# Kernel tuning notes

Measured on AMD Instinct MI355X. Metric: run time of the kernel, lower is better.

The kernel has to match this reference:

```python
import jax, jax.numpy as jnp
import numpy as np

EPS = 1e-6
NUM_HEADS = 12


def ln_cf(x, w, b):
    # channels_first LayerNorm over channel dim (ConvNeXt style)
    u = jnp.mean(x, axis=1, keepdims=True)
    s = jnp.mean((x - u) ** 2, axis=1, keepdims=True)
    xn = (x - u) / jnp.sqrt(s + EPS)
    shp = (1, -1) + (1,) * (x.ndim - 2)
    return xn * w.reshape(shp) + b.reshape(shp)


def conv2s2(x, w):
    # Conv3d kernel=2 stride=2 (no bias): exact non-overlapping patch contraction
    b, c, H, W, D = x.shape
    xp = x.reshape(b, c, H // 2, 2, W // 2, 2, D // 2, 2)
    return jnp.einsum('bchkwpdq,ockpq->bohwd', xp, w)


def convt2s2(x, w):
    # ConvTranspose3d kernel=2 stride=2 (torch weight layout [in, out, 2,2,2])
    b, i, H, W, D = x.shape
    o = w.shape[1]
    y = jnp.einsum('bihwd,iokpq->bohkwpdq', x, w)
    return y.reshape(b, o, 2 * H, 2 * W, 2 * D)


def stem(x, w1, g1, b1, w2, g2, b2):
    h = conv2s2(x, w1)
    h = jax.nn.gelu(ln_cf(h, g1, b1), approximate=False)
    h = conv2s2(h, w2)
    return ln_cf(h, g2, b2)


def debed(x, tw1, g, b, tw2, tb2):
    h = convt2s2(x, tw1)
    h = jax.nn.gelu(ln_cf(h, g, b), approximate=False)
    return convt2s2(h, tw2) + tb2.reshape(1, -1, 1, 1, 1)


def rope(x):
    # rotary embedding over full token dim c (pairs (i, i+c/2)), positions 0..L-1
    b, l, c = x.shape
    inv = 1.0 / (10000.0 ** (jnp.arange(0, c, 2, dtype=jnp.float32) / c))
    t = jnp.arange(l, dtype=jnp.float32)
    f = jnp.outer(t, inv)                      # [l, c/2]
    emb = jnp.concatenate([f, f], axis=-1)     # [l, c]
    cos, sin = jnp.cos(emb)[None], jnp.sin(emb)[None]
    rot = jnp.concatenate([-x[..., c // 2:], x[..., :c // 2]], axis=-1)
    return x * cos + rot * sin


def _forward(x, skip, q_w1, q_g1, q_b1, q_w2, q_g2, q_b2,
             k_w1, k_g1, k_b1, k_w2, k_g2, k_b2,
             v_w1, v_g1, v_b1, v_w2, v_g2, v_b2,
             o_tw1, o_g, o_b, o_tw2, o_tb2,
             ns_w, ns_b, nx_w, nx_b, no_w, no_b):
    res = skip
    skip = ln_cf(skip, ns_w, ns_b)
    x = ln_cf(x, nx_w, nx_b)
    q = stem(skip, q_w1, q_g1, q_b1, q_w2, q_g2, q_b2)
    k = stem(x, k_w1, k_g1, k_b1, k_w2, k_g2, k_b2)
    v = stem(x, v_w1, v_g1, v_b1, v_w2, v_g2, v_b2)
    b, c, Hq, Wq, Dq = q.shape
    _, _, Hk, Wk, Dk = k.shape
    q = q.reshape(b, c, -1).transpose(0, 2, 1)   # [b, Lq, c]
    k = k.reshape(b, c, -1).transpose(0, 2, 1)   # [b, Lk, c]
    v = v.reshape(b, c, -1).transpose(0, 2, 1)
    q = rope(q)
    k = rope(k)
    hd = c // NUM_HEADS
    qh = q.reshape(b, -1, NUM_HEADS, hd).transpose(0, 2, 1, 3)  # [b, nh, Lq, hd]
    kh = k.reshape(b, -1, NUM_HEADS, hd).transpose(0, 2, 1, 3)
    vh = v.reshape(b, -1, NUM_HEADS, hd).transpose(0, 2, 1, 3)
    scale = 1.0 / jnp.sqrt(jnp.float32(hd))
    attn = jax.nn.softmax(jnp.einsum('bhqc,bhkc->bhqk', qh, kh) * scale, axis=-1)
    proj = jnp.einsum('bhqk,bhkc->bhqc', attn, vh)              # [b, nh, Lq, hd]
    # rearrange 'b nh l c -> b (c nh) h w d'
    proj = proj.transpose(0, 3, 1, 2).reshape(b, c, Hq, Wq, Dq)
    proj = ln_cf(proj, no_w, no_b)
    out = debed(proj, o_tw1, o_g, o_b, o_tw2, o_tb2)
    return out + res


def setup_inputs() -> dict:
    key = jax.random.key(0)
    ks = iter(jax.random.split(key, 40))
    def nrm(shape, scale):
        return jax.random.normal(next(ks), shape, jnp.float32) * scale
    E, E4, XF, SF = 768, 192, 6, 6
    inp = {
        'x': nrm((2, XF, 48, 48, 48), 1.0),
        'skip': nrm((2, SF, 48, 48, 48), 1.0),
    }
    for p, ic in [('q', SF), ('k', XF), ('v', XF)]:
        inp[p + '_w1'] = nrm((E4, ic, 2, 2, 2), (ic * 8) ** -0.5)
        inp[p + '_g1'] = jnp.ones(E4, jnp.float32)
        inp[p + '_b1'] = jnp.zeros(E4, jnp.float32)
        inp[p + '_w2'] = nrm((E, E4, 2, 2, 2), (E4 * 8) ** -0.5)
        inp[p + '_g2'] = jnp.ones(E, jnp.float32)
        inp[p + '_b2'] = jnp.zeros(E, jnp.float32)
    inp['o_tw1'] = nrm((E, E4, 2, 2, 2), E ** -0.5)
    inp['o_g'] = jnp.ones(E4, jnp.float32)
    inp['o_b'] = jnp.zeros(E4, jnp.float32)
    inp['o_tw2'] = nrm((E4, SF, 2, 2, 2), E4 ** -0.5)
    inp['o_tb2'] = jnp.zeros(SF, jnp.float32)
    inp['ns_w'] = jnp.ones(SF, jnp.float32)
    inp['ns_b'] = jnp.zeros(SF, jnp.float32)
    inp['nx_w'] = jnp.ones(XF, jnp.float32)
    inp['nx_b'] = jnp.zeros(XF, jnp.float32)
    inp['no_w'] = jnp.ones(E, jnp.float32)
    inp['no_b'] = jnp.zeros(E, jnp.float32)
    return inp


def reference(x, skip, q_w1, q_g1, q_b1, q_w2, q_g2, q_b2,
              k_w1, k_g1, k_b1, k_w2, k_g2, k_b2,
              v_w1, v_g1, v_b1, v_w2, v_g2, v_b2,
              o_tw1, o_g, o_b, o_tw2, o_tb2,
              ns_w, ns_b, nx_w, nx_b, no_w, no_b):
    return _forward(x, skip, q_w1, q_g1, q_b1, q_w2, q_g2, q_b2,
                    k_w1, k_g1, k_b1, k_w2, k_g2, k_b2,
                    v_w1, v_g1, v_b1, v_w2, v_g2, v_b2,
                    o_tw1, o_g, o_b, o_tw2, o_tb2,
                    ns_w, ns_b, nx_w, nx_b, no_w, no_b)
```

## Files before the change

### kernel.cpp

```cpp
#include <hip/hip_runtime.h>
#include <math.h>

#define BB_ 2
#define C0 6
#define S0 48
#define V0 (S0*S0*S0)
#define C1 192
#define S1 24
#define V1 (S1*S1*S1)
#define C2 768
#define S2 12
#define LL (S2*S2*S2)
#define NH 12
#define HD 64
#define KDIM (C1*8)
#define MDIM (BB_*LL)

typedef __attribute__((ext_vector_type(8))) short short8;
typedef __attribute__((ext_vector_type(4))) short short4v;
typedef __attribute__((ext_vector_type(4))) float float4v;

static __device__ __forceinline__ float gelu_exact(float x){
  return 0.5f*x*(1.0f+erff(x*0.70710678118654752440f));
}
static __device__ __forceinline__ unsigned short f2bf(float f){
  unsigned int u = __float_as_uint(f);
  unsigned int r = (u + 0x7fffu + ((u>>16)&1u)) >> 16;
  return (unsigned short)r;
}
static __device__ __forceinline__ unsigned int pk_bf16(float a, float b){
#if __has_builtin(__builtin_amdgcn_cvt_pk_bf16_f32)
  typedef __attribute__((ext_vector_type(2))) __bf16 bf2;
  bf2 r = __builtin_amdgcn_cvt_pk_bf16_f32(a,b);
  union { bf2 v; unsigned int u; } cv; cv.v = r;
  return cv.u;
#else
  return (unsigned int)f2bf(a) | ((unsigned int)f2bf(b)<<16);
#endif
}
static __device__ __forceinline__ float bf2f(unsigned short u){
  return __uint_as_float(((unsigned int)u)<<16);
}
static __device__ __forceinline__ float exp2v(float x){
#if __has_builtin(__builtin_amdgcn_exp2f)
  return __builtin_amdgcn_exp2f(x);
#else
  return exp2f(x);
#endif
}
static __device__ __forceinline__ void load_lds16(const void* g, void* l){
  __builtin_amdgcn_global_load_lds((const __attribute__((address_space(1))) unsigned int*)g,
      (__attribute__((address_space(3))) unsigned int*)l, 16, 0, 0);
}
static __device__ __forceinline__ float4v mfma32(short8 a, short8 b, float4v c){
  return __builtin_amdgcn_mfma_f32_16x16x32_bf16(a,b,c,0,0,0);
}
static __device__ __forceinline__ float4v mfma16(short4v a, short4v b, float4v c){
#if __has_builtin(__builtin_amdgcn_mfma_f32_16x16x16bf16_1k)
  return __builtin_amdgcn_mfma_f32_16x16x16bf16_1k(a,b,c,0,0,0);
#else
  asm volatile("v_mfma_f32_16x16x16_bf16 %0, %1, %2, %0" : "+v"(c) : "v"(a), "v"(b));
  return c;
#endif
}

__global__ __launch_bounds__(256) void prep_kernel(
    const float* __restrict__ skin, const float* __restrict__ xin,
    const float* __restrict__ nsw, const float* __restrict__ nsb,
    const float* __restrict__ nxw, const float* __restrict__ nxb,
    unsigned short* __restrict__ outS, unsigned short* __restrict__ outX,
    const float* __restrict__ qw2, const float* __restrict__ kw2, const float* __restrict__ vw2,
    const float* __restrict__ tw1, const float* __restrict__ tw2,
    const float* __restrict__ qw1, const float* __restrict__ kw1, const float* __restrict__ vw1,
    unsigned short* __restrict__ w2tq, unsigned short* __restrict__ w2tk,
    unsigned short* __restrict__ w2tv, unsigned short* __restrict__ Btd,
    unsigned short* __restrict__ Bt48,
    unsigned short* __restrict__ w1q, unsigned short* __restrict__ w1k,
    unsigned short* __restrict__ w1v){
  int bx = blockIdx.x;
  if (bx < 1728){
    int z = bx >= 864;
    const float* in = z ? xin : skin;
    const float* w  = z ? nxw : nsw;
    const float* bi = z ? nxb : nsb;
    unsigned short* out = z ? outX : outS;
    int idx = (bx - z*864)*256 + threadIdx.x;
    int b = idx / V0, vox = idx - b*V0;
    const float* p = in + (size_t)b*(C0*V0) + vox;
    float v[C0]; float s=0.f;
#pragma unroll
    for (int c=0;c<C0;c++){ v[c]=p[(size_t)c*V0]; s+=v[c]; }
    float u = s*(1.f/C0);
    float ss=0.f;
#pragma unroll
    for (int c=0;c<C0;c++){ float d=v[c]-u; ss+=d*d; }
    float inv = rsqrtf(ss*(1.f/C0)+1e-6f);
    unsigned short* o = out + (size_t)b*(C0*V0) + vox;
#pragma unroll
    for (int c=0;c<C0;c++) o[(size_t)c*V0] = f2bf((v[c]-u)*inv*w[c]+bi[c]);
    return;
  }
  bx -= 1728;
  if (bx < 13824){
    int z = bx/4608;
    int idx = (bx - z*4608)*256 + threadIdx.x;
    const float* w2 = (z==0)?qw2:((z==1)?kw2:vw2);
    unsigned short* o = (z==0)?w2tq:((z==1)?w2tk:w2tv);
    int oc = idx/KDIM; int r = idx-oc*KDIM; int p = r/C1; int ic = r-p*C1;
    o[idx] = f2bf(w2[(size_t)oc*KDIM + ic*8 + p]);
  } else if (bx < 18432){
    int idx = (bx-13824)*256 + threadIdx.x;
    int n = idx/C2; int p = idx-n*C2;
    int i = ((p&63)*NH) + (p>>6);
    int kpq = n/C1, o2 = n-kpq*C1;
    Btd[idx] = f2bf(tw1[(size_t)i*KDIM + o2*8 + kpq]);
  } else if (bx < 18480){
    int idx = (bx-18432)*256 + threadIdx.x;
    int n = idx/C1; int i = idx-n*C1;
    Bt48[idx] = (n<48) ? f2bf(tw2[(size_t)i*48 + n]) : (unsigned short)0;
  } else {
    int idx = (bx-18480)*256 + threadIdx.x;
    int z = idx / 9216; int r = idx - z*9216;
    const float* w1 = (z==0)?qw1:((z==1)?kw1:vw1);
    unsigned short* o = (z==0)?w1q:((z==1)?w1k:w1v);
    o[r] = f2bf(w1[r]);
  }
}

__global__ __launch_bounds__(256) void conv1_kernel(
    const unsigned short* __restrict__ lnSb, const unsigned short* __restrict__ lnXb,
    const unsigned short* __restrict__ w1bq, const unsigned short* __restrict__ w1bk,
    const unsigned short* __restrict__ w1bv,
    const float* __restrict__ qg1, const float* __restrict__ qb1,
    const float* __restrict__ kg1, const float* __restrict__ kb1,
    const float* __restrict__ vg1, const float* __restrict__ vb1,
    unsigned short* __restrict__ h1q, unsigned short* __restrict__ h1k,
    unsigned short* __restrict__ h1v){
  int z = blockIdx.z;
  const unsigned short* in = (z==0)? lnSb : lnXb;
  const unsigned short* Wb = (z==0)?w1bq:((z==1)?w1bk:w1bv);
  const float* g1 = (z==0)?qg1:((z==1)?kg1:vg1);
  const float* b1 = (z==0)?qb1:((z==1)?kb1:vb1);
  unsigned short* h1p = (z==0)?h1q:((z==1)?h1k:h1v);
  int t = threadIdx.x, w = t>>6, lane = t&63;
  int g = lane>>4, l16 = lane&15;
  int j = blockIdx.x*4 + w;
  int bxh = j/18, mt = j - bxh*18;
  int b = bxh/48; int rem = bxh - b*48; int y = rem>>1, xh = rem&1;
  int xo = mt/3, zo = mt - xo*3;
  int xv = xh*12 + xo*2 + (l16>>3);
  int zv = zo*8 + (l16&7);
  int x2 = 2*xv, z2 = 2*zv, y2 = 2*y;
  const unsigned short* base = in + (size_t)b*C0*V0;
  union { short8 v; unsigned int u[4]; } aA;
  {
    size_t rb = (size_t)g*V0;
    aA.u[0] = *(const unsigned int*)&base[rb + (y2+0)*(S0*S0) + (x2+0)*S0 + z2];
    aA.u[1] = *(const unsigned int*)&base[rb + (y2+0)*(S0*S0) + (x2+1)*S0 + z2];
    aA.u[2] = *(const unsigned int*)&base[rb + (y2+1)*(S0*S0) + (x2+0)*S0 + z2];
    aA.u[3] = *(const unsigned int*)&base[rb + (y2+1)*(S0*S0) + (x2+1)*S0 + z2];
  }
  union { short4v v; unsigned int u[2]; } aB;
  {
    size_t rb = (size_t)(4+(g>>1))*V0 + (y2+(g&1))*(S0*S0);
    aB.u[0] = *(const unsigned int*)&base[rb + (x2+0)*S0 + z2];
    aB.u[1] = *(const unsigned int*)&base[rb + (x2+1)*S0 + z2];
  }
  float4v acc[12];
#pragma unroll
  for (int ot=0; ot<12; ot++){
    short8  wA = *(const short8*)&Wb[(ot*16+l16)*48 + g*8];
    short4v wB = *(const short4v*)&Wb[(ot*16+l16)*48 + 32 + g*4];
    float4v a = {};
    a = mfma32(wA, aA.v, a);
    a = mfma16(wB, aB.v, a);
    acc[ot] = a;
  }
  float s1=0.f, s2=0.f;
#pragma unroll
  for (int ot=0;ot<12;ot++)
#pragma unroll
    for (int reg=0;reg<4;reg++){ float v=acc[ot][reg]; s1+=v; s2+=v*v; }
  s1 += __shfl_xor(s1,16); s1 += __shfl_xor(s1,32);
  s2 += __shfl_xor(s2,16); s2 += __shfl_xor(s2,32);
  float u = s1*(1.f/C1);
  float inv = rsqrtf(s2*(1.f/C1)-u*u+1e-6f);
  int tok = (y>>1)*(S2*S2) + (xv>>1)*S2 + (zv>>1);
  int p8 = (y&1)*4 + (xv&1)*2 + (zv&1);
  unsigned short* hb = h1p + (size_t)(b*LL+tok)*KDIM + p8*C1;
#pragma unroll
  for (int ot=0; ot<12; ot++){
    int oc0 = ot*16 + g*4;
    float4 gg = *(const float4*)&g1[oc0];
    float4 bb = *(const float4*)&b1[oc0];
    float x0 = gelu_exact((acc[ot][0]-u)*inv*gg.x+bb.x);
    float x1 = gelu_exact((acc[ot][1]-u)*inv*gg.y+bb.y);
    float x2e= gelu_exact((acc[ot][2]-u)*inv*gg.z+bb.z);
    float x3 = gelu_exact((acc[ot][3]-u)*inv*gg.w+bb.w);
    uint2 pk; pk.x = pk_bf16(x0,x1); pk.y = pk_bf16(x2e,x3);
    *(uint2*)&hb[oc0] = pk;
  }
}

__global__ __launch_bounds__(256) void gemm_stem_kernel(
    const unsigned short* __restrict__ A0, const unsigned short* __restrict__ A1,
    const unsigned short* __restrict__ A2,
    const unsigned short* __restrict__ B0, const unsigned short* __restrict__ B1,
    const unsigned short* __restrict__ B2,
    unsigned short* __restrict__ Cq, unsigned short* __restrict__ Ck,
    unsigned short* __restrict__ Cv){
  int flat = blockIdx.x;
  int xcd = flat & 7, slot = flat >> 3;
  int tile = xcd*122 + slot;
  if (tile >= 972) return;
  int z = tile/324; int rr = tile - z*324;
  int m0 = (rr/12)*128, n0 = (rr - (rr/12)*12)*64;
  const unsigned short* A = (z==0)?A0:((z==1)?A1:A2);
  const unsigned short* Bt = (z==0)?B0:((z==1)?B1:B2);
  unsigned short* Cp = (z==0)?Cq:((z==1)?Ck:Cv);
  __shared__ __align__(16) unsigned short Al[2][128*32];
  __shared__ __align__(16) unsigned short Bl[2][64*32];
  int t=threadIdx.x, w=t>>6, lane=t&63;
  int g=lane>>4, l16=lane&15, r16=lane>>2, c16=lane&3;
  int wm=w>>1, wn=w&1;
  int csrc = (c16 ^ ((r16>>1)&3))*8;
  int crd  = (g   ^ ((l16>>1)&3))*8;
  float4v acc[4][2] = {};
#pragma unroll
  for (int cc=0;cc<3;cc++){
    int ch = w*3+cc;
    if (ch<8) load_lds16(A + (size_t)(m0+ch*16+r16)*KDIM + csrc, &Al[0][ch*512]);
    else      load_lds16(Bt + (size_t)(n0+(ch-8)*16+r16)*KDIM + csrc, &Bl[0][(ch-8)*512]);
  }
  __syncthreads();
  int cur = 0;
  for (int kb=0;kb<KDIM;kb+=32){
    if (kb+32 < KDIM){
      int nb = cur^1;
#pragma unroll
      for (int cc=0;cc<3;cc++){
        int ch = w*3+cc;
        if (ch<8) load_lds16(A + (size_t)(m0+ch*16+r16)*KDIM + (kb+32) + csrc, &Al[nb][ch*512]);
        else      load_lds16(Bt + (size_t)(n0+(ch-8)*16+r16)*KDIM + (kb+32) + csrc, &Bl[nb][(ch-8)*512]);
      }
    }
    short8 af[4], bf[2];
#pragma unroll
    for (int mt=0;mt<4;mt++) af[mt] = *(const short8*)&Al[cur][(wm*64+mt*16+l16)*32 + crd];
#pragma unroll
    for (int nt=0;nt<2;nt++) bf[nt] = *(const short8*)&Bl[cur][(wn*32+nt*16+l16)*32 + crd];
#pragma unroll
    for (int mt=0;mt<4;mt++)
#pragma unroll
      for (int nt=0;nt<2;nt++)
        acc[mt][nt] = mfma32(af[mt], bf[nt], acc[mt][nt]);
    __syncthreads();
    cur ^= 1;
  }
#pragma unroll
  for (int mt=0;mt<4;mt++){
    int mb = m0 + wm*64 + mt*16 + g*4;
#pragma unroll
    for (int nt=0;nt<2;nt++){
      int col = n0 + wn*32 + nt*16 + l16;
#pragma unroll
      for (int reg=0;reg<4;reg++)
        Cp[(size_t)(mb+reg)*C2 + col] = f2bf(acc[mt][nt][reg]);
    }
  }
}

__global__ __launch_bounds__(256) void gemm_debed_kernel(const unsigned short* __restrict__ A,
    const unsigned short* __restrict__ Bt, unsigned short* __restrict__ C){
  int flat = blockIdx.x;
  int xcd = flat & 7, slot = flat >> 3;
  int tile = xcd*81 + slot;
  int m0 = (tile/24)*128, n0 = (tile - (tile/24)*24)*64;
  __shared__ __align__(16) unsigned short Al[2][128*32];
  __shared__ __align__(16) unsigned short Bl[2][64*32];
  int t=threadIdx.x, w=t>>6, lane=t&63;
  int g=lane>>4, l16=lane&15, r16=lane>>2, c16=lane&3;
  int wm=w>>1, wn=w&1;
  int csrc = (c16 ^ ((r16>>1)&3))*8;
  int crd  = (g   ^ ((l16>>1)&3))*8;
  float4v acc[4][2] = {};
#pragma unroll
  for (int cc=0;cc<3;cc++){
    int ch = w*3+cc;
    if (ch<8) load_lds16(A + (size_t)(m0+ch*16+r16)*C2 + csrc, &Al[0][ch*512]);
    else      load_lds16(Bt + (size_t)(n0+(ch-8)*16+r16)*C2 + csrc, &Bl[0][(ch-8)*512]);
  }
  __syncthreads();
  int cur = 0;
  for (int kb=0;kb<C2;kb+=32){
    if (kb+32 < C2){
      int nb = cur^1;
#pragma unroll
      for (int cc=0;cc<3;cc++){
        int ch = w*3+cc;
        if (ch<8) load_lds16(A + (size_t)(m0+ch*16+r16)*C2 + (kb+32) + csrc, &Al[nb][ch*512]);
        else      load_lds16(Bt + (size_t)(n0+(ch-8)*16+r16)*C2 + (kb+32) + csrc, &Bl[nb][(ch-8)*512]);
      }
    }
    short8 af[4], bf[2];
#pragma unroll
    for (int mt=0;mt<4;mt++) af[mt] = *(const short8*)&Al[cur][(wm*64+mt*16+l16)*32 + crd];
#pragma unroll
    for (int nt=0;nt<2;nt++) bf[nt] = *(const short8*)&Bl[cur][(wn*32+nt*16+l16)*32 + crd];
#pragma unroll
    for (int mt=0;mt<4;mt++)
#pragma unroll
      for (int nt=0;nt<2;nt++)
        acc[mt][nt] = mfma32(af[mt], bf[nt], acc[mt][nt]);
    __syncthreads();
    cur ^= 1;
  }
#pragma unroll
  for (int nt=0;nt<2;nt++){
    int n = n0 + wn*32 + nt*16 + l16;
    int kpq = n / C1;
    int o = n - kpq*C1;
#pragma unroll
    for (int mt=0;mt<4;mt++){
      int mb = m0 + wm*64 + mt*16 + g*4;
#pragma unroll
      for (int reg=0;reg<4;reg++){
        int m = mb + reg;
        int b = m / LL; int tok = m - b*LL;
        int h = tok/(S2*S2), ww=(tok/S2)%S2, d=tok%S2;
        int v24 = (2*h+((kpq>>2)&1))*(S1*S1) + (2*ww+((kpq>>1)&1))*S1 + (2*d+(kpq&1));
        C[(size_t)(b*V1+v24)*C1 + o] = f2bf(acc[mt][nt][reg]);
      }
    }
  }
}

__global__ __launch_bounds__(256) void final_kernel(const unsigned short* __restrict__ dh,
    const unsigned short* __restrict__ Bt48, const float* __restrict__ og,
    const float* __restrict__ ob, const float* __restrict__ tb2s,
    const float* __restrict__ skipp, float* __restrict__ out){
  __shared__ __align__(16) unsigned short As[64*200];
  __shared__ __align__(16) unsigned short Bs[64*200];
  int t=threadIdx.x, w=t>>6, lane=t&63;
  int g=lane>>4, l16=lane&15;
  int m0 = blockIdx.x*64;
  for (int n8 = t; n8 < 1536; n8 += 256){
    int n64 = n8/24, kk = (n8 - n64*24)*8;
    uint4 d4 = *(const uint4*)&Bt48[n64*192 + kk];
    *(uint4*)&Bs[n64*200 + kk] = d4;
  }
  float g0=og[lane], g1v=og[lane+64], g2v=og[lane+128];
  float b0=ob[lane], b1v=ob[lane+64], b2v=ob[lane+128];
  for (int rr=0; rr<16; rr++){
    int rl = w*16 + rr;
    const unsigned short* row = dh + (size_t)(m0+rl)*C1;
    float v0=bf2f(row[lane]), v1=bf2f(row[lane+64]), v2=bf2f(row[lane+128]);
    float s1=v0+v1+v2, s2=v0*v0+v1*v1+v2*v2;
#pragma unroll
    for (int off=32;off>0;off>>=1){ s1+=__shfl_xor(s1,off); s2+=__shfl_xor(s2,off); }
    float u=s1*(1.f/C1), inv=rsqrtf(s2*(1.f/C1)-u*u+1e-6f);
    As[rl*200+lane]     = f2bf(gelu_exact((v0-u)*inv*g0+b0));
    As[rl*200+lane+64]  = f2bf(gelu_exact((v1-u)*inv*g1v+b1v));
    As[rl*200+lane+128] = f2bf(gelu_exact((v2-u)*inv*g2v+b2v));
  }
  __syncthreads();
  int wm=w>>1, wn=w&1;
  float4v acc[2][2] = {};
#pragma unroll
  for (int kb=0;kb<192;kb+=32){
    short8 af[2], bf[2];
#pragma unroll
    for (int mt=0;mt<2;mt++) af[mt] = *(const short8*)&As[(wm*32+mt*16+l16)*200 + kb + g*8];
#pragma unroll
    for (int nt=0;nt<2;nt++) bf[nt] = *(const short8*)&Bs[(wn*32+nt*16+l16)*200 + kb + g*8];
#pragma unroll
    for (int mt=0;mt<2;mt++)
#pragma unroll
      for (int nt=0;nt<2;nt++)
        acc[mt][nt] = mfma32(af[mt], bf[nt], acc[mt][nt]);
  }
#pragma unroll
  for (int nt=0;nt<2;nt++){
    int n = wn*32 + nt*16 + l16;
    if (n < 48){
      int c = n>>3, kpq = n&7;
      float bias = tb2s[c];
#pragma unroll
      for (int mt=0;mt<2;mt++){
        int mb = m0 + wm*32 + mt*16 + g*4;
#pragma unroll
        for (int reg=0;reg<4;reg++){
          int m = mb + reg;
          int b = m / V1; int v24 = m - b*V1;
          int y24 = v24/(S1*S1), x24=(v24/S1)%S1, z24=v24%S1;
          int vox = (2*y24+((kpq>>2)&1))*(S0*S0) + (2*x24+((kpq>>1)&1))*S0 + 2*z24+(kpq&1);
          size_t oi = (size_t)(b*C0+c)*V0 + vox;
          out[oi] = acc[mt][nt][reg] + bias + skipp[oi];
        }
      }
    }
  }
}

__global__ __launch_bounds__(256) void ln768_stem_kernel(
    unsigned short* __restrict__ qb, unsigned short* __restrict__ kb2,
    unsigned short* __restrict__ vb,
    const float* __restrict__ qg, const float* __restrict__ qbi,
    const float* __restrict__ kg, const float* __restrict__ kbi,
    const float* __restrict__ vg, const float* __restrict__ vbi, float qscale){
  int z = blockIdx.y;
  unsigned short* buf = (z==0)?qb:((z==1)?kb2:vb);
  const float* g  = (z==0)?qg:((z==1)?kg:vg);
  const float* bia= (z==0)?qbi:((z==1)?kbi:vbi);
  float scale = (z==0)? qscale : 1.0f;
  int tok = blockIdx.x*4 + (threadIdx.x>>6), lane = threadIdx.x&63;
  unsigned short* row = buf + (size_t)tok*C2;
  float v[12]; float s1=0.f,s2=0.f;
#pragma unroll
  for (int i=0;i<12;i++){ float t=bf2f(row[i*64+lane]); v[i]=t; s1+=t; s2+=t*t; }
#pragma unroll
  for (int off=32;off>0;off>>=1){ s1+=__shfl_xor(s1,off); s2+=__shfl_xor(s2,off); }
  float u=s1*(1.f/C2);
  float inv=rsqrtf(s2*(1.f/C2)-u*u+1e-6f);
  if (z==2){
#pragma unroll
    for (int i=0;i<12;i++){ int j=i*64+lane; row[j]=f2bf((v[i]-u)*inv*g[j]+bia[j]); }
  } else {
    int pos = tok % LL;
#pragma unroll
    for (int i=0;i<6;i++){
      int j=i*64+lane;
      float xn1=(v[i]-u)*inv*g[j]+bia[j];
      float xn2=(v[i+6]-u)*inv*g[j+384]+bia[j+384];
      float fr=(float)pos*__expf(-0.02398526139f*(float)j);
      float cs=cosf(fr), sn=sinf(fr);
      row[j]     = f2bf((xn1*cs - xn2*sn)*scale);
      row[j+384] = f2bf((xn2*cs + xn1*sn)*scale);
    }
  }
}

__global__ __launch_bounds__(256) void vtrans_kernel(const unsigned short* __restrict__ vbf,
    unsigned short* __restrict__ vT){
  __shared__ unsigned short T[64*72];
  int tok0 = blockIdx.x*64;
  int h = blockIdx.y, b = blockIdx.z;
  int t = threadIdx.x;
#pragma unroll
  for (int i=0;i<2;i++){
    int idx = t + i*256;
    int token = idx>>3, dc = idx&7;
    uint4 d4 = *(const uint4*)&vbf[(size_t)(b*LL+tok0+token)*C2 + h*64 + dc*8];
    const unsigned short* s = (const unsigned short*)&d4;
#pragma unroll
    for (int j2=0;j2<8;j2++) T[(dc*8+j2)*72 + token] = s[j2];
  }
  __syncthreads();
  int r = t>>2, seg = t&3;
  unsigned short* dst = vT + (size_t)((b*NH+h)*HD + r)*LL + tok0 + seg*16;
  uint4 o[2];
  unsigned short* os = (unsigned short*)o;
#pragma unroll
  for (int j2=0;j2<16;j2++) os[j2] = T[r*72 + seg*16 + j2];
  *(uint4*)dst = o[0];
  *(uint4*)(dst+8) = o[1];
}

__global__ __launch_bounds__(256) void attn_kernel(const unsigned short* __restrict__ q,
    const unsigned short* __restrict__ k, const unsigned short* __restrict__ vt,
    unsigned short* __restrict__ opart, float* __restrict__ lbuf){
  __shared__ __align__(16) unsigned char smem[32768];
  unsigned short* Ks = (unsigned short*)smem;
  unsigned short* Vs = Ks + 4096;
  int flat = blockIdx.x;
  int xcd = flat & 7, slot = flat >> 3;
  int tile = xcd*108 + slot;
  int h = tile / 72; int rem = tile - h*72;
  int zb = rem / 9, qt = rem - zb*9;
  int b = zb >> 2, split = zb & 3;
  int t=threadIdx.x, w=t>>6, lane=t&63;
  int g=lane>>4, l16=lane&15;
  short8 qA[3], qB[3];
#pragma unroll
  for (int j=0;j<3;j++){
    const unsigned short* qrow = q + (size_t)(b*LL + qt*192 + w*48 + j*16 + l16)*C2 + h*64;
    qA[j] = *(const short8*)(qrow + g*8);
    qB[j] = *(const short8*)(qrow + 32 + g*8);
  }
  const unsigned short* kbase = k + (size_t)(b*LL)*C2 + h*64;
  const unsigned short* vbase = vt + (size_t)((b*NH+h)*HD)*LL;
  int sub = lane>>3;
  int chs = (lane&7) ^ sub;
  int ktb = split*7, kte = (split==3)? 27 : (split*7+7);
  const unsigned short* gptr[4];
  unsigned short* ldst[4];
  int gstep[4];
#pragma unroll
  for (int cc=0;cc<4;cc++){
    int ii = w*4+cc;
    if (ii<8){
      int key = ktb*64 + ii*8 + sub;
      gptr[cc] = kbase + (size_t)key*C2 + chs*8;
      gstep[cc] = 64*C2;
      ldst[cc] = &Ks[ii*512];
    } else {
      int d = (ii-8)*8 + sub;
      gptr[cc] = vbase + (size_t)d*LL + ktb*64 + chs*8;
      gstep[cc] = 64;
      ldst[cc] = &Vs[(ii-8)*512];
    }
  }
  int sw = l16 & 7;
  const unsigned short* ksrow = &Ks[l16*64 + (g^sw)*8];
  int c2d = (((4+g)^sw) - (g^sw))*8;
  const unsigned short* vsrow = &Vs[l16*64 + (g&1)*4];
  int xk[4];
#pragma unroll
  for (int kc=0;kc<4;kc++) xk[kc] = (((kc*2 + (g>>1)) ^ sw))*8;
  short4v vones;
  vones[0]=vones[1]=vones[2]=vones[3]=(short)0x3F80;
  float4v O4[3][4] = {};
  float4v Ol[3] = {};
#pragma unroll
  for (int cc=0;cc<4;cc++){
    load_lds16(gptr[cc], ldst[cc]);
    gptr[cc] += gstep[cc];
  }
  __syncthreads();
  int cur = 0;
  for (int kt=ktb; kt<kte; kt++){
    if (kt+1 < kte){
      int so = (cur^1)*8192;
#pragma unroll
      for (int cc=0;cc<4;cc++){
        load_lds16(gptr[cc], ldst[cc]+so);
        gptr[cc] += gstep[cc];
      }
    }
    int co = cur*8192;
    const unsigned short* kr = ksrow + co;
    const unsigned short* vr = vsrow + co;
    float4v sc[3][4];
#pragma unroll
    for (int nt=0;nt<4;nt++){
      short8 k1 = *(const short8*)(kr + nt*1024);
      short8 k2 = *(const short8*)(kr + nt*1024 + c2d);
#pragma unroll
      for (int j=0;j<3;j++){
        float4v zz = {};
        zz = mfma32(k1, qA[j], zz);
        zz = mfma32(k2, qB[j], zz);
        sc[j][nt] = zz;
      }
    }
#pragma unroll
    for (int j=0;j<3;j++)
#pragma unroll
      for (int nt=0;nt<4;nt++)
#pragma unroll
        for (int reg=0;reg<4;reg++)
          sc[j][nt][reg] = exp2v(sc[j][nt][reg]);
    short4v pbs[3][4];
#pragma unroll
    for (int j=0;j<3;j++)
#pragma unroll
      for (int kc=0;kc<4;kc++){
        union { short4v v; unsigned int u[2]; } pb;
        pb.u[0] = pk_bf16(sc[j][kc][0], sc[j][kc][1]);
        pb.u[1] = pk_bf16(sc[j][kc][2], sc[j][kc][3]);
        pbs[j][kc] = pb.v;
      }
#pragma unroll
    for (int kc=0;kc<4;kc++){
      const unsigned short* vp = vr + xk[kc];
      short4v va[4];
#pragma unroll
      for (int dt=0;dt<4;dt++) va[dt] = *(const short4v*)(vp + dt*1024);
#pragma unroll
      for (int j=0;j<3;j++){
        Ol[j] = mfma16(vones, pbs[j][kc], Ol[j]);
#pragma unroll
        for (int dt=0;dt<4;dt++)
          O4[j][dt] = mfma16(va[dt], pbs[j][kc], O4[j][dt]);
      }
    }
    __syncthreads();
    cur ^= 1;
  }
  float* Ot = (float*)smem;
  float* ot = Ot + w*1216;
  int qq = lane>>2, c4 = lane&3;
#pragma unroll
  for (int j=0;j<3;j++){
#pragma unroll
    for (int dt=0;dt<4;dt++)
      *(float4*)&ot[l16*76 + dt*16 + g*4] =
          make_float4(O4[j][dt][0],O4[j][dt][1],O4[j][dt][2],O4[j][dt][3]);
    if (g==0){
      int qi = qt*192 + w*48 + j*16 + l16;
      lbuf[((size_t)(b*4+split)*NH+h)*LL + qi] = Ol[j][0];
    }
    unsigned short* orow = opart + (size_t)split*MDIM*C2
                + (size_t)(b*LL + qt*192 + w*48 + j*16 + qq)*C2 + h*64;
#pragma unroll
    for (int p=0;p<4;p++){
      float4 vv = *(float4*)&ot[qq*76 + p*16 + c4*4];
      uint2 pk; pk.x = pk_bf16(vv.x,vv.y); pk.y = pk_bf16(vv.z,vv.w);
      *(uint2*)&orow[p*16 + c4*4] = pk;
    }
    __syncthreads();
  }
}

__global__ __launch_bounds__(256) void attn_post_kernel(const unsigned short* __restrict__ opart,
    const float* __restrict__ lbuf,
    const float* __restrict__ g, const float* __restrict__ bia,
    unsigned short* __restrict__ aob){
  int t=threadIdx.x, w=t>>6, lane=t&63;
  int m = blockIdx.x*4 + w;
  int b = m / LL, l = m - b*LL;
  const unsigned short* o0 = opart + (size_t)m*C2;
  unsigned short* orow = aob + (size_t)m*C2;
  float vv[12]; float s1=0.f, s2=0.f;
#pragma unroll
  for (int i=0;i<12;i++){
    float ls = 0.f;
#pragma unroll
    for (int s=0;s<4;s++) ls += lbuf[((size_t)(b*4+s)*NH+i)*LL + l];
    float inv = 1.f/ls;
    int j = i*64+lane;
    float val = 0.f;
#pragma unroll
    for (int s=0;s<4;s++) val += bf2f(o0[(size_t)s*MDIM*C2 + j]);
    val *= inv;
    vv[i]=val; s1+=val; s2+=val*val;
  }
#pragma unroll
  for (int off=32;off>0;off>>=1){ s1+=__shfl_xor(s1,off); s2+=__shfl_xor(s2,off); }
  float u=s1*(1.f/C2);
  float invs=rsqrtf(s2*(1.f/C2)-u*u+1e-6f);
#pragma unroll
  for (int i=0;i<12;i++){
    int cj = lane*NH + i;
    orow[i*64+lane] = f2bf((vv[i]-u)*invs*g[cj]+bia[cj]);
  }
}

extern "C" void kernel_launch(void* const* d_in, const int* in_sizes, int n_in,
                              void* d_out, int out_size, void* d_ws, size_t ws_size,
                              hipStream_t stream){
  (void)in_sizes; (void)n_in; (void)out_size; (void)ws_size;
  const float* x    =(const float*)d_in[0];
  const float* skip =(const float*)d_in[1];
  const float* q_w1 =(const float*)d_in[2];
  const float* q_g1 =(const float*)d_in[3];
  const float* q_b1 =(const float*)d_in[4];
  const float* q_w2 =(const float*)d_in[5];
  const float* q_g2 =(const float*)d_in[6];
  const float* q_b2 =(const float*)d_in[7];
  const float* k_w1 =(const float*)d_in[8];
  const float* k_g1 =(const float*)d_in[9];
  const float* k_b1 =(const float*)d_in[10];
  const float* k_w2 =(const float*)d_in[11];
  const float* k_g2 =(const float*)d_in[12];
  const float* k_b2 =(const float*)d_in[13];
  const float* v_w1 =(const float*)d_in[14];
  const float* v_g1 =(const float*)d_in[15];
  const float* v_b1 =(const float*)d_in[16];
  const float* v_w2 =(const float*)d_in[17];
  const float* v_g2 =(const float*)d_in[18];
  const float* v_b2 =(const float*)d_in[19];
  const float* o_tw1=(const float*)d_in[20];
  const float* o_g  =(const float*)d_in[21];
  const float* o_b  =(const float*)d_in[22];
  const float* o_tw2=(const float*)d_in[23];
  const float* o_tb2=(const float*)d_in[24];
  const float* ns_w =(const float*)d_in[25];
  const float* ns_b =(const float*)d_in[26];
  const float* nx_w =(const float*)d_in[27];
  const float* nx_b =(const float*)d_in[28];
  const float* no_w =(const float*)d_in[29];
  const float* no_b =(const float*)d_in[30];
  float* out=(float*)d_out;

  char* W = (char*)d_ws;
  unsigned short* lnSb = (unsigned short*)(W + 0);
  unsigned short* lnXb = (unsigned short*)(W + 2654208);
  unsigned short* h1q  = (unsigned short*)(W + 5308416);
  unsigned short* h1k  = (unsigned short*)(W + 15925248);
  unsigned short* h1v  = (unsigned short*)(W + 26542080);
  unsigned short* w2tq = (unsigned short*)(W + 37158912);
  unsigned short* w2tk = (unsigned short*)(W + 39518208);
  unsigned short* w2tv = (unsigned short*)(W + 41877504);
  unsigned short* qbf  = (unsigned short*)(W + 44236800);
  unsigned short* kbf  = (unsigned short*)(W + 49545216);
  unsigned short* vbf  = (unsigned short*)(W + 54853632);
  unsigned short* vT   = (unsigned short*)(W + 60162048);
  unsigned short* aob  = (unsigned short*)(W + 65470464);
  unsigned short* Btd  = (unsigned short*)(W + 70778880);
  unsigned short* Bt48 = (unsigned short*)(W + 73138176);
  unsigned short* w1q  = (unsigned short*)(W + 73162752);
  unsigned short* w1k  = (unsigned short*)(W + 73181184);
  unsigned short* w1v  = (unsigned short*)(W + 73199616);
  float* lbuf  = (float*)(W + 0);
  unsigned short* opart = (unsigned short*)(W + 5308416);
  unsigned short* dh   = (unsigned short*)(W + 5308416);

  const float QSCALE = 0.125f*1.44269504089f;

  prep_kernel<<<20316,256,0,stream>>>(skip, x, ns_w, ns_b, nx_w, nx_b, lnSb, lnXb,
      q_w2,k_w2,v_w2,o_tw1,o_tw2, q_w1,k_w1,v_w1,
      w2tq,w2tk,w2tv,Btd,Bt48, w1q,w1k,w1v);
  conv1_kernel<<<dim3(432,1,3),256,0,stream>>>(lnSb,lnXb, w1q,w1k,w1v,
      q_g1,q_b1, k_g1,k_b1, v_g1,v_b1, h1q,h1k,h1v);
  gemm_stem_kernel<<<976,256,0,stream>>>(h1q,h1k,h1v,
      w2tq,w2tk,w2tv, qbf,kbf,vbf);
  ln768_stem_kernel<<<dim3(864,3),256,0,stream>>>(qbf,kbf,vbf,
      q_g2,q_b2, k_g2,k_b2, v_g2,v_b2, QSCALE);
  vtrans_kernel<<<dim3(27,12,2),256,0,stream>>>(vbf, vT);
  attn_kernel<<<864,256,0,stream>>>(qbf, kbf, vT, opart, lbuf);
  attn_post_kernel<<<864,256,0,stream>>>(opart, lbuf, no_w, no_b, aob);
  gemm_debed_kernel<<<648,256,0,stream>>>(aob, Btd, dh);
  final_kernel<<<432,256,0,stream>>>(dh, Bt48, o_g, o_b, o_tb2, skip, out);
}
```

Baseline: 326.3 us.

## Triple-buffer LDS staging in stem and debed GEMMs with vmcnt-based waits

Both the stem and debed bf16 GEMM kernels move from double-buffered to triple-buffered LDS tiles. The global-to-LDS load for a tile two steps ahead is issued before the current tile's MFMAs. Each iteration now waits with s_waitcnt vmcnt(3) plus a raw s_barrier instead of a full __syncthreads that drains all loads. This keeps one tile of loads in flight across the barrier to hide global latency, at the cost of 50% more LDS per block (possibly lowering occupancy) and reliance on exact vmcnt counting.

```diff
diff --git a/kernel.cpp b/kernel.cpp
--- a/kernel.cpp
+++ b/kernel.cpp
@@ -218,45 +218,58 @@
   const unsigned short* A = (z==0)?A0:((z==1)?A1:A2);
   const unsigned short* Bt = (z==0)?B0:((z==1)?B1:B2);
   unsigned short* Cp = (z==0)?Cq:((z==1)?Ck:Cv);
-  __shared__ __align__(16) unsigned short Al[2][128*32];
-  __shared__ __align__(16) unsigned short Bl[2][64*32];
+  __shared__ __align__(16) unsigned short Al[3][128*32];
+  __shared__ __align__(16) unsigned short Bl[3][64*32];
   int t=threadIdx.x, w=t>>6, lane=t&63;
   int g=lane>>4, l16=lane&15, r16=lane>>2, c16=lane&3;
   int wm=w>>1, wn=w&1;
   int csrc = (c16 ^ ((r16>>1)&3))*8;
   int crd  = (g   ^ ((l16>>1)&3))*8;
   float4v acc[4][2] = {};
-#pragma unroll
-  for (int cc=0;cc<3;cc++){
-    int ch = w*3+cc;
-    if (ch<8) load_lds16(A + (size_t)(m0+ch*16+r16)*KDIM + csrc, &Al[0][ch*512]);
-    else      load_lds16(Bt + (size_t)(n0+(ch-8)*16+r16)*KDIM + csrc, &Bl[0][(ch-8)*512]);
-  }
-  __syncthreads();
-  int cur = 0;
-  for (int kb=0;kb<KDIM;kb+=32){
-    if (kb+32 < KDIM){
-      int nb = cur^1;
-#pragma unroll
-      for (int cc=0;cc<3;cc++){
-        int ch = w*3+cc;
-        if (ch<8) load_lds16(A + (size_t)(m0+ch*16+r16)*KDIM + (kb+32) + csrc, &Al[nb][ch*512]);
-        else      load_lds16(Bt + (size_t)(n0+(ch-8)*16+r16)*KDIM + (kb+32) + csrc, &Bl[nb][(ch-8)*512]);
-      }
-    }
+  auto STAGE = [&](int buf, int kcol){
+#pragma unroll
+    for (int cc=0;cc<3;cc++){
+      int ch = w*3+cc;
+      if (ch<8) load_lds16(A + (size_t)(m0+ch*16+r16)*KDIM + kcol + csrc, &Al[buf][ch*512]);
+      else      load_lds16(Bt + (size_t)(n0+(ch-8)*16+r16)*KDIM + kcol + csrc, &Bl[buf][(ch-8)*512]);
+    }
+  };
+  auto COMPUTE = [&](int buf){
     short8 af[4], bf[2];
 #pragma unroll
-    for (int mt=0;mt<4;mt++) af[mt] = *(const short8*)&Al[cur][(wm*64+mt*16+l16)*32 + crd];
-#pragma unroll
-    for (int nt=0;nt<2;nt++) bf[nt] = *(const short8*)&Bl[cur][(wn*32+nt*16+l16)*32 + crd];
+    for (int mt=0;mt<4;mt++) af[mt] = *(const short8*)&Al[buf][(wm*64+mt*16+l16)*32 + crd];
+#pragma unroll
+    for (int nt=0;nt<2;nt++) bf[nt] = *(const short8*)&Bl[buf][(wn*32+nt*16+l16)*32 + crd];
 #pragma unroll
     for (int mt=0;mt<4;mt++)
 #pragma unroll
       for (int nt=0;nt<2;nt++)
         acc[mt][nt] = mfma32(af[mt], bf[nt], acc[mt][nt]);
-    __syncthreads();
-    cur ^= 1;
-  }
+  };
+  const int NT = KDIM/32;
+  STAGE(0, 0);
+  STAGE(1, 32);
+  asm volatile("s_waitcnt vmcnt(3)" ::: "memory");
+  __builtin_amdgcn_s_barrier();
+  __builtin_amdgcn_sched_barrier(0);
+  int cur = 0;
+  for (int tt=0; tt<NT-2; tt++){
+    int nb = cur+2; if (nb>=3) nb-=3;
+    STAGE(nb, tt*32+64);
+    COMPUTE(cur);
+    __builtin_amdgcn_sched_barrier(0);
+    asm volatile("s_waitcnt vmcnt(3)" ::: "memory");
+    __builtin_amdgcn_s_barrier();
+    __builtin_amdgcn_sched_barrier(0);
+    cur++; if (cur>=3) cur-=3;
+  }
+  COMPUTE(cur);
+  __builtin_amdgcn_sched_barrier(0);
+  asm volatile("s_waitcnt vmcnt(0)" ::: "memory");
+  __builtin_amdgcn_s_barrier();
+  __builtin_amdgcn_sched_barrier(0);
+  cur++; if (cur>=3) cur-=3;
+  COMPUTE(cur);
 #pragma unroll
   for (int mt=0;mt<4;mt++){
     int mb = m0 + wm*64 + mt*16 + g*4;
@@ -276,45 +289,58 @@
   int xcd = flat & 7, slot = flat >> 3;
   int tile = xcd*81 + slot;
   int m0 = (tile/24)*128, n0 = (tile - (tile/24)*24)*64;
-  __shared__ __align__(16) unsigned short Al[2][128*32];
-  __shared__ __align__(16) unsigned short Bl[2][64*32];
+  __shared__ __align__(16) unsigned short Al[3][128*32];
+  __shared__ __align__(16) unsigned short Bl[3][64*32];
   int t=threadIdx.x, w=t>>6, lane=t&63;
   int g=lane>>4, l16=lane&15, r16=lane>>2, c16=lane&3;
   int wm=w>>1, wn=w&1;
   int csrc = (c16 ^ ((r16>>1)&3))*8;
   int crd  = (g   ^ ((l16>>1)&3))*8;
   float4v acc[4][2] = {};
-#pragma unroll
-  for (int cc=0;cc<3;cc++){
-    int ch = w*3+cc;
-    if (ch<8) load_lds16(A + (size_t)(m0+ch*16+r16)*C2 + csrc, &Al[0][ch*512]);
-    else      load_lds16(Bt + (size_t)(n0+(ch-8)*16+r16)*C2 + csrc, &Bl[0][(ch-8)*512]);
-  }
-  __syncthreads();
-  int cur = 0;
-  for (int kb=0;kb<C2;kb+=32){
-    if (kb+32 < C2){
-      int nb = cur^1;
-#pragma unroll
-      for (int cc=0;cc<3;cc++){
-        int ch = w*3+cc;
-        if (ch<8) load_lds16(A + (size_t)(m0+ch*16+r16)*C2 + (kb+32) + csrc, &Al[nb][ch*512]);
-        else      load_lds16(Bt + (size_t)(n0+(ch-8)*16+r16)*C2 + (kb+32) + csrc, &Bl[nb][(ch-8)*512]);
-      }
-    }
+  auto STAGE = [&](int buf, int kcol){
+#pragma unroll
+    for (int cc=0;cc<3;cc++){
+      int ch = w*3+cc;
+      if (ch<8) load_lds16(A + (size_t)(m0+ch*16+r16)*C2 + kcol + csrc, &Al[buf][ch*512]);
+      else      load_lds16(Bt + (size_t)(n0+(ch-8)*16+r16)*C2 + kcol + csrc, &Bl[buf][(ch-8)*512]);
+    }
+  };
+  auto COMPUTE = [&](int buf){
     short8 af[4], bf[2];
 #pragma unroll
-    for (int mt=0;mt<4;mt++) af[mt] = *(const short8*)&Al[cur][(wm*64+mt*16+l16)*32 + crd];
-#pragma unroll
-    for (int nt=0;nt<2;nt++) bf[nt] = *(const short8*)&Bl[cur][(wn*32+nt*16+l16)*32 + crd];
+    for (int mt=0;mt<4;mt++) af[mt] = *(const short8*)&Al[buf][(wm*64+mt*16+l16)*32 + crd];
+#pragma unroll
+    for (int nt=0;nt<2;nt++) bf[nt] = *(const short8*)&Bl[buf][(wn*32+nt*16+l16)*32 + crd];
 #pragma unroll
     for (int mt=0;mt<4;mt++)
 #pragma unroll
       for (int nt=0;nt<2;nt++)
         acc[mt][nt] = mfma32(af[mt], bf[nt], acc[mt][nt]);
-    __syncthreads();
-    cur ^= 1;
-  }
+  };
+  const int NT = C2/32;
+  STAGE(0, 0);
+  STAGE(1, 32);
+  asm volatile("s_waitcnt vmcnt(3)" ::: "memory");
+  __builtin_amdgcn_s_barrier();
+  __builtin_amdgcn_sched_barrier(0);
+  int cur = 0;
+  for (int tt=0; tt<NT-2; tt++){
+    int nb = cur+2; if (nb>=3) nb-=3;
+    STAGE(nb, tt*32+64);
+    COMPUTE(cur);
+    __builtin_amdgcn_sched_barrier(0);
+    asm volatile("s_waitcnt vmcnt(3)" ::: "memory");
+    __builtin_amdgcn_s_barrier();
+    __builtin_amdgcn_sched_barrier(0);
+    cur++; if (cur>=3) cur-=3;
+  }
+  COMPUTE(cur);
+  __builtin_amdgcn_sched_barrier(0);
+  asm volatile("s_waitcnt vmcnt(0)" ::: "memory");
+  __builtin_amdgcn_s_barrier();
+  __builtin_amdgcn_sched_barrier(0);
+  cur++; if (cur>=3) cur-=3;
+  COMPUTE(cur);
 #pragma unroll
   for (int nt=0;nt<2;nt++){
     int n = n0 + wn*32 + nt*16 + l16;
```

After: 324.9 us. About the same (-0.4%).
